# Optimization experiments

Hardware: AMD Instinct MI355X
Metric: run time of the kernel (lower is better)

The kernel has to match this reference:

```python
import jax, jax.numpy as jnp
import numpy as np

VOCAB, EMB, HID, LAYERS = 50000, 128, 128, 3
B, T = 4096, 50


def gru_layer(x, Wih, Whh, bih, bhh):
    """PyTorch-convention GRU over time-major x: [T, B, D] -> [T, B, H]."""
    H = Whh.shape[1]
    h0 = jnp.zeros((x.shape[1], H), x.dtype)
    gi_all = jnp.einsum('tbd,gd->tbg', x, Wih) + bih  # precompute input gates [T,B,3H]

    def step(h, gi):
        gh = h @ Whh.T + bhh
        i_r, i_z, i_n = jnp.split(gi, 3, axis=-1)
        h_r, h_z, h_n = jnp.split(gh, 3, axis=-1)
        r = jax.nn.sigmoid(i_r + h_r)
        z = jax.nn.sigmoid(i_z + h_z)
        n = jnp.tanh(i_n + r * h_n)
        h_new = (1.0 - z) * n + z * h
        return h_new, h_new

    _, ys = jax.lax.scan(step, h0, gi_all)
    return ys


def drnn(x, params):
    """Dilated RNN stack (zalandoresearch DRNN): dilation 2^l per layer.
    x: [B, T, E] -> [B, T, H]."""
    h = jnp.swapaxes(x, 0, 1)  # time-major [T, B, D]
    for l, (Wih, Whh, bih, bhh) in enumerate(params):
        rate = 2 ** l
        Tn, Bn, Dn = h.shape
        Tp = ((Tn + rate - 1) // rate) * rate
        hp = jnp.pad(h, ((0, Tp - Tn), (0, 0), (0, 0)))
        # interleave: dilated[t', j*B:(j+1)*B] = hp[t'*rate + j]
        hd = hp.reshape(Tp // rate, rate * Bn, Dn)
        od = gru_layer(hd, Wih, Whh, bih, bhh)  # [Tp/rate, rate*B, H]
        h = od.reshape(Tp, Bn, -1)[:Tn]
    return jnp.swapaxes(h, 0, 1)  # [B, T, H]


def setup_inputs() -> dict:
    key = jax.random.key(0)
    ks = jax.random.split(key, 2 + 4 * LAYERS)
    inp = {}
    inp['text_inputs'] = jax.random.randint(ks[0], (B, T), 0, VOCAB)
    inp['mask_input'] = (inp['text_inputs'] > 0).astype(jnp.int32)
    inp['len_seq'] = inp['mask_input'].sum(axis=1)
    inp['emb'] = jax.random.normal(ks[1], (VOCAB, EMB), jnp.float32) * 0.02
    s = 1.0 / np.sqrt(HID)
    for l in range(LAYERS):
        din = EMB if l == 0 else HID
        k0, k1, k2, k3 = ks[2 + 4 * l], ks[3 + 4 * l], ks[4 + 4 * l], ks[5 + 4 * l]
        inp[f'Wih{l}'] = jax.random.uniform(k0, (3 * HID, din), jnp.float32, -s, s)
        inp[f'Whh{l}'] = jax.random.uniform(k1, (3 * HID, HID), jnp.float32, -s, s)
        inp[f'bih{l}'] = jax.random.uniform(k2, (3 * HID,), jnp.float32, -s, s)
        inp[f'bhh{l}'] = jax.random.uniform(k3, (3 * HID,), jnp.float32, -s, s)
    return inp


def reference(text_inputs, mask_input, len_seq, emb,
              Wih0, Whh0, bih0, bhh0,
              Wih1, Whh1, bih1, bhh1,
              Wih2, Whh2, bih2, bhh2):
    params = [(Wih0, Whh0, bih0, bhh0),
              (Wih1, Whh1, bih1, bhh1),
              (Wih2, Whh2, bih2, bhh2)]
    x = emb[text_inputs]                       # [B, T, E]
    lens = jnp.sign(text_inputs).sum(axis=1)   # recomputed mask lengths
    order = jnp.argsort(-lens)                 # sort descending by length
    inv = jnp.argsort(order)                   # inverse permutation
    out = drnn(x[order], params)[inv]          # [B, T, H]
    sent_mask = (lens > 0).astype(out.dtype)   # zero out empty sentences
    return out * sent_mask[:, None, None]
```

## Files before the change

### kernel.cpp

```cpp
#include <hip/hip_runtime.h>
#include <hip/hip_bf16.h>
#include <hip/hip_fp16.h>
#include <math.h>


#define B_N 4096
#define T_N 50
#define H_N 128

typedef _Float16 half8 __attribute__((ext_vector_type(8)));
typedef float f32x4 __attribute__((ext_vector_type(4)));

__global__ void prep_weights_kernel(const float* __restrict__ Wih,
                                    const float* __restrict__ Whh,
                                    const float* __restrict__ bih,
                                    const float* __restrict__ bhh,
                                    _Float16* __restrict__ Wp,
                                    float* __restrict__ biasP) {
  const int g = blockIdx.x;
  const int k = threadIdx.x;
  Wp[g * H_N + k]         = (_Float16)Wih[(size_t)g * H_N + k];
  Wp[49152 + g * H_N + k] = (_Float16)Whh[(size_t)g * H_N + k];
  if (k == 0) {
    if (g < 256) biasP[g] = bih[g] + bhh[g];
    else { biasP[g] = bih[g]; biasP[g + 128] = bhh[g]; }
  }
}

__global__ void gather_kernel(const int* __restrict__ tok,
                              const float* __restrict__ emb,
                              _Float16* __restrict__ X0) {
  const int tid = threadIdx.x;
  const int r   = blockIdx.x * 16 + (tid >> 4);
  const int t   = r >> 12;
  const int b   = r & (B_N - 1);
  const int c8  = (tid & 15) * 8;
  const int tk  = tok[b * T_N + t];
  const float4* ep = (const float4*)(emb + (size_t)tk * H_N + c8);
  const float4 a = ep[0], d = ep[1];
  half8 v = { (_Float16)a.x, (_Float16)a.y, (_Float16)a.z, (_Float16)a.w,
              (_Float16)d.x, (_Float16)d.y, (_Float16)d.z, (_Float16)d.w };
  *(half8*)(X0 + (size_t)r * H_N + c8) = v;
}

__global__ void mask_kernel(const int* __restrict__ tok, float* __restrict__ mask) {
  const int b = blockIdx.x * 256 + threadIdx.x;
  int any = 0;
  for (int t = 0; t < T_N; ++t) any |= tok[b * T_N + t];
  mask[b] = any ? 1.0f : 0.0f;
}

__device__ __forceinline__ float sigm(float x) {
  return 1.0f / (1.0f + __expf(-x));
}
__device__ __forceinline__ float tanh_fast(float x) {
  x = fminf(fmaxf(x, -15.0f), 15.0f);
  const float t = __expf(2.0f * x);
  return (t - 1.0f) / (t + 1.0f);
}

template <int RATE, int TSTEPS, bool LAST>
__global__ __launch_bounds__(512, 2) void gru_mfma_kernel(
    const _Float16* __restrict__ X, void* __restrict__ Yv,
    const _Float16* __restrict__ Wp, const float* __restrict__ biasP,
    const float* __restrict__ maskF) {
  __shared__ _Float16 hs[2][16][136];

  const int tid  = threadIdx.x;
  const int lane = tid & 63;
  const int w    = tid >> 6;
  const int cb   = w * 16;
  const int l15  = lane & 15;
  const int lq   = lane >> 4;
  const int c    = cb + l15;

  {
    _Float16* hp = &hs[0][0][0];
    for (int i = tid; i < 16 * 136; i += 512) hp[i] = (_Float16)0.f;
  }

  half8 Wf[3][4], Uf[3][4];
#pragma unroll
  for (int g = 0; g < 3; ++g)
#pragma unroll
    for (int kc = 0; kc < 4; ++kc) {
      const size_t off = (size_t)(g * H_N + c) * H_N + kc * 32 + lq * 8;
      Wf[g][kc] = *(const half8*)(Wp + off);
      Uf[g][kc] = *(const half8*)(Wp + 49152 + off);
    }

  const float br = biasP[c],       bz = biasP[128 + c];
  const float bi = biasP[256 + c], bh = biasP[384 + c];
  float hold[4] = {0.f, 0.f, 0.f, 0.f};

  const int d0 = blockIdx.x * 16;

  half8 xc[4], xn[4];
  {
    const _Float16* xp = X + ((size_t)d0 + l15) * H_N + lq * 8;
#pragma unroll
    for (int kc = 0; kc < 4; ++kc) xc[kc] = *(const half8*)(xp + kc * 32);
  }
  __syncthreads();

  for (int tp = 0; tp < TSTEPS; ++tp) {
    const int cur = tp & 1, nxt = cur ^ 1;

    {
      const int tn = (tp + 1 < TSTEPS) ? tp + 1 : tp;
      const _Float16* xp =
          X + ((size_t)tn * RATE * B_N + d0 + l15) * H_N + lq * 8;
#pragma unroll
      for (int kc = 0; kc < 4; ++kc) xn[kc] = *(const half8*)(xp + kc * 32);
    }

    half8 hf[4];
#pragma unroll
    for (int kc = 0; kc < 4; ++kc)
      hf[kc] = *(const half8*)(&hs[cur][l15][kc * 32 + lq * 8]);

    f32x4 ar  = {br, br, br, br}, az  = {bz, bz, bz, bz};
    f32x4 ani = {bi, bi, bi, bi}, anh = {bh, bh, bh, bh};
#pragma unroll
    for (int kc = 0; kc < 4; ++kc) {
      ar  = __builtin_amdgcn_mfma_f32_16x16x32_f16(xc[kc], Wf[0][kc], ar,  0, 0, 0);
      az  = __builtin_amdgcn_mfma_f32_16x16x32_f16(xc[kc], Wf[1][kc], az,  0, 0, 0);
      ani = __builtin_amdgcn_mfma_f32_16x16x32_f16(xc[kc], Wf[2][kc], ani, 0, 0, 0);
      ar  = __builtin_amdgcn_mfma_f32_16x16x32_f16(hf[kc], Uf[0][kc], ar,  0, 0, 0);
      az  = __builtin_amdgcn_mfma_f32_16x16x32_f16(hf[kc], Uf[1][kc], az,  0, 0, 0);
      anh = __builtin_amdgcn_mfma_f32_16x16x32_f16(hf[kc], Uf[2][kc], anh, 0, 0, 0);
    }

#pragma unroll
    for (int j = 0; j < 4; ++j) {
      const int crow = lq * 4 + j;
      const float rr = sigm(ar[j]);
      const float zz = sigm(az[j]);
      const float nn = tanh_fast(ani[j] + rr * anh[j]);
      const float hv = nn + zz * (hold[j] - nn);
      hold[j] = hv;

      const _Float16 hhalf = (_Float16)hv;
      const unsigned short hb = __builtin_bit_cast(unsigned short, hhalf);
      const unsigned int other =
          (unsigned short)__shfl_xor((int)hb, 1, 64);
      const unsigned int packed = (unsigned int)hb | (other << 16);

      if (!(lane & 1))
        *(unsigned int*)(&hs[nxt][crow][c]) = packed;

      if (!LAST) {
        if (!(lane & 1)) {
          const size_t row_g = (size_t)tp * RATE * B_N + d0 + crow;
          *(unsigned int*)((_Float16*)Yv + row_g * H_N + c) = packed;
        }
      } else {
        const int d = d0 + crow;
        const int t = tp * RATE + (d >> 12);
        if (t < T_N) {
          const int b = d & (B_N - 1);
          ((float*)Yv)[((size_t)b * T_N + t) * H_N + c] = hv * maskF[b];
        }
      }
    }

#pragma unroll
    for (int kc = 0; kc < 4; ++kc) xc[kc] = xn[kc];
    __syncthreads();
  }
}

extern "C" void kernel_launch(void* const* d_in, const int* in_sizes, int n_in,
                              void* d_out, int out_size, void* d_ws, size_t ws_size,
                              hipStream_t stream) {
  (void)in_sizes; (void)n_in; (void)out_size; (void)ws_size;
  const int*   tok = (const int*)d_in[0];
  const float* emb = (const float*)d_in[3];

  char* ws = (char*)d_ws;
  const size_t XBYTES = (size_t)212992 * H_N * 2;
  _Float16* X0    = (_Float16*)ws;
  _Float16* X1    = (_Float16*)(ws + XBYTES);
  _Float16* Wp    = (_Float16*)(ws + 2 * XBYTES);
  float*    biasP = (float*)(ws + 2 * XBYTES + 3 * 196608);
  float*    maskF = biasP + 3 * 512;

  for (int l = 0; l < 3; ++l) {
    const float* Wih = (const float*)d_in[4 + 4 * l];
    const float* Whh = (const float*)d_in[5 + 4 * l];
    const float* bih = (const float*)d_in[6 + 4 * l];
    const float* bhh = (const float*)d_in[7 + 4 * l];
    prep_weights_kernel<<<384, 128, 0, stream>>>(Wih, Whh, bih, bhh,
                                                 Wp + (size_t)l * 98304,
                                                 biasP + l * 512);
  }
  gather_kernel<<<12800, 256, 0, stream>>>(tok, emb, X0);
  mask_kernel<<<16, 256, 0, stream>>>(tok, maskF);
  hipMemsetAsync(X0 + (size_t)204800 * H_N, 0,
                 (size_t)(212992 - 204800) * H_N * 2, stream);

  gru_mfma_kernel<1, 50, false><<<256, 512, 0, stream>>>(
      X0, X1, Wp, biasP, maskF);
  gru_mfma_kernel<2, 25, false><<<512, 512, 0, stream>>>(
      X1, X0, Wp + 98304, biasP + 512, maskF);
  gru_mfma_kernel<4, 13, true><<<1024, 512, 0, stream>>>(
      X0, (float*)d_out, Wp + 2 * 98304, biasP + 1024, maskF);
}
```

Baseline: 464.1 us.

## Store activations and weights in MFMA fragment layout, batch input projections per 4 steps

Weights and activations are pre-swizzled into MFMA fragment order so each lane loads a contiguous half8, and the recurrent weights are staged in LDS (about 104 KB dynamic shared memory) instead of registers. The input projection for four timesteps is computed in one batch before the sequential recurrence, which moves it off the serial critical path and frees registers. The cost is more LDS traffic per step for U fragments, lower occupancy from the large LDS allocation, and scalar 16-bit stores for h.

After: 530.5 us. +14.3%, slower.

```diff
diff --git a/kernel.cpp b/kernel.cpp
--- a/kernel.cpp
+++ b/kernel.cpp
@@ -11,16 +11,23 @@
 typedef _Float16 half8 __attribute__((ext_vector_type(8)));
 typedef float f32x4 __attribute__((ext_vector_type(4)));
 
+#define MFMA16(a, b, c) __builtin_amdgcn_mfma_f32_16x16x32_f16((a), (b), (c), 0, 0, 0)
+
 __global__ void prep_weights_kernel(const float* __restrict__ Wih,
                                     const float* __restrict__ Whh,
                                     const float* __restrict__ bih,
                                     const float* __restrict__ bhh,
-                                    _Float16* __restrict__ Wp,
+                                    _Float16* __restrict__ WihF,
+                                    _Float16* __restrict__ WhhF,
                                     float* __restrict__ biasP) {
   const int g = blockIdx.x;
   const int k = threadIdx.x;
-  Wp[g * H_N + k]         = (_Float16)Wih[(size_t)g * H_N + k];
-  Wp[49152 + g * H_N + k] = (_Float16)Whh[(size_t)g * H_N + k];
+  const int gate = g >> 7, c = g & 127;
+  const int wv = c >> 4, kc = k >> 5;
+  const int lane = (c & 15) | (((k >> 3) & 3) << 4);
+  const int idx = ((wv * 12 + gate * 4 + kc) * 64 + lane) * 8 + (k & 7);
+  WihF[idx] = (_Float16)Wih[(size_t)g * H_N + k];
+  WhhF[idx] = (_Float16)Whh[(size_t)g * H_N + k];
   if (k == 0) {
     if (g < 256) biasP[g] = bih[g] + bhh[g];
     else { biasP[g] = bih[g]; biasP[g + 128] = bhh[g]; }
@@ -29,18 +36,21 @@
 
 __global__ void gather_kernel(const int* __restrict__ tok,
                               const float* __restrict__ emb,
-                              _Float16* __restrict__ X0) {
-  const int tid = threadIdx.x;
-  const int r   = blockIdx.x * 16 + (tid >> 4);
-  const int t   = r >> 12;
-  const int b   = r & (B_N - 1);
-  const int c8  = (tid & 15) * 8;
-  const int tk  = tok[b * T_N + t];
+                              _Float16* __restrict__ XF) {
+  const int p    = blockIdx.x;
+  const int tid  = threadIdx.x;
+  const int kc   = tid >> 6;
+  const int lane = tid & 63;
+  const int row  = p * 16 + (lane & 15);
+  const int t    = row >> 12;
+  const int b    = row & (B_N - 1);
+  const int c8   = kc * 32 + (lane >> 4) * 8;
+  const int tk   = tok[b * T_N + t];
   const float4* ep = (const float4*)(emb + (size_t)tk * H_N + c8);
   const float4 a = ep[0], d = ep[1];
   half8 v = { (_Float16)a.x, (_Float16)a.y, (_Float16)a.z, (_Float16)a.w,
               (_Float16)d.x, (_Float16)d.y, (_Float16)d.z, (_Float16)d.w };
-  *(half8*)(X0 + (size_t)r * H_N + c8) = v;
+  *(half8*)(XF + (((size_t)p * 4 + kc) * 64 + lane) * 8) = v;
 }
 
 __global__ void mask_kernel(const int* __restrict__ tok, float* __restrict__ mask) {
@@ -61,114 +71,121 @@
 
 template <int RATE, int TSTEPS, bool LAST>
 __global__ __launch_bounds__(512, 2) void gru_mfma_kernel(
-    const _Float16* __restrict__ X, void* __restrict__ Yv,
-    const _Float16* __restrict__ Wp, const float* __restrict__ biasP,
-    const float* __restrict__ maskF) {
-  __shared__ _Float16 hs[2][16][136];
+    const _Float16* __restrict__ XF, void* __restrict__ Yv,
+    const _Float16* __restrict__ WihF, const _Float16* __restrict__ WhhF,
+    const float* __restrict__ biasP, const float* __restrict__ maskF) {
+  extern __shared__ _Float16 lds[];
+  _Float16* Ul  = lds;
+  _Float16* hsl = lds + 49152;
 
   const int tid  = threadIdx.x;
   const int lane = tid & 63;
   const int w    = tid >> 6;
-  const int cb   = w * 16;
   const int l15  = lane & 15;
   const int lq   = lane >> 4;
-  const int c    = cb + l15;
-
-  {
-    _Float16* hp = &hs[0][0][0];
-    for (int i = tid; i < 16 * 136; i += 512) hp[i] = (_Float16)0.f;
-  }
-
-  half8 Wf[3][4], Uf[3][4];
-#pragma unroll
-  for (int g = 0; g < 3; ++g)
-#pragma unroll
-    for (int kc = 0; kc < 4; ++kc) {
-      const size_t off = (size_t)(g * H_N + c) * H_N + kc * 32 + lq * 8;
-      Wf[g][kc] = *(const half8*)(Wp + off);
-      Uf[g][kc] = *(const half8*)(Wp + 49152 + off);
-    }
+  const int c    = (w << 4) + l15;
+  const int d0   = blockIdx.x << 4;
+
+  for (int i = tid; i < 6144; i += 512)
+    *(half8*)(Ul + i * 8) = *(const half8*)(WhhF + (size_t)i * 8);
+  for (int i = tid; i < 512; i += 512)
+    *(half8*)(hsl + i * 8) = half8{0,0,0,0,0,0,0,0};
 
   const float br = biasP[c],       bz = biasP[128 + c];
   const float bi = biasP[256 + c], bh = biasP[384 + c];
+  float mkv[4];
+#pragma unroll
+  for (int j = 0; j < 4; ++j)
+    mkv[j] = LAST ? maskF[(d0 & (B_N - 1)) + lq * 4 + j] : 0.0f;
+
   float hold[4] = {0.f, 0.f, 0.f, 0.f};
-
-  const int d0 = blockIdx.x * 16;
-
-  half8 xc[4], xn[4];
-  {
-    const _Float16* xp = X + ((size_t)d0 + l15) * H_N + lq * 8;
-#pragma unroll
-    for (int kc = 0; kc < 4; ++kc) xc[kc] = *(const half8*)(xp + kc * 32);
-  }
   __syncthreads();
 
-  for (int tp = 0; tp < TSTEPS; ++tp) {
-    const int cur = tp & 1, nxt = cur ^ 1;
-
-    {
-      const int tn = (tp + 1 < TSTEPS) ? tp + 1 : tp;
-      const _Float16* xp =
-          X + ((size_t)tn * RATE * B_N + d0 + l15) * H_N + lq * 8;
-#pragma unroll
-      for (int kc = 0; kc < 4; ++kc) xn[kc] = *(const half8*)(xp + kc * 32);
+  int cur = 0;
+  for (int tp0 = 0; tp0 < TSTEPS; tp0 += 4) {
+    const int bs = (TSTEPS - tp0 < 4) ? (TSTEPS - tp0) : 4;
+
+    f32x4 gr[4], gz[4], gn[4];
+#pragma unroll
+    for (int s = 0; s < 4; ++s) {
+      gr[s] = f32x4{br, br, br, br};
+      gz[s] = f32x4{bz, bz, bz, bz};
+      gn[s] = f32x4{bi, bi, bi, bi};
     }
-
-    half8 hf[4];
-#pragma unroll
-    for (int kc = 0; kc < 4; ++kc)
-      hf[kc] = *(const half8*)(&hs[cur][l15][kc * 32 + lq * 8]);
-
-    f32x4 ar  = {br, br, br, br}, az  = {bz, bz, bz, bz};
-    f32x4 ani = {bi, bi, bi, bi}, anh = {bh, bh, bh, bh};
 #pragma unroll
     for (int kc = 0; kc < 4; ++kc) {
-      ar  = __builtin_amdgcn_mfma_f32_16x16x32_f16(xc[kc], Wf[0][kc], ar,  0, 0, 0);
-      az  = __builtin_amdgcn_mfma_f32_16x16x32_f16(xc[kc], Wf[1][kc], az,  0, 0, 0);
-      ani = __builtin_amdgcn_mfma_f32_16x16x32_f16(xc[kc], Wf[2][kc], ani, 0, 0, 0);
-      ar  = __builtin_amdgcn_mfma_f32_16x16x32_f16(hf[kc], Uf[0][kc], ar,  0, 0, 0);
-      az  = __builtin_amdgcn_mfma_f32_16x16x32_f16(hf[kc], Uf[1][kc], az,  0, 0, 0);
-      anh = __builtin_amdgcn_mfma_f32_16x16x32_f16(hf[kc], Uf[2][kc], anh, 0, 0, 0);
-    }
-
-#pragma unroll
-    for (int j = 0; j < 4; ++j) {
-      const int crow = lq * 4 + j;
-      const float rr = sigm(ar[j]);
-      const float zz = sigm(az[j]);
-      const float nn = tanh_fast(ani[j] + rr * anh[j]);
-      const float hv = nn + zz * (hold[j] - nn);
-      hold[j] = hv;
-
-      const _Float16 hhalf = (_Float16)hv;
-      const unsigned short hb = __builtin_bit_cast(unsigned short, hhalf);
-      const unsigned int other =
-          (unsigned short)__shfl_xor((int)hb, 1, 64);
-      const unsigned int packed = (unsigned int)hb | (other << 16);
-
-      if (!(lane & 1))
-        *(unsigned int*)(&hs[nxt][crow][c]) = packed;
-
-      if (!LAST) {
-        if (!(lane & 1)) {
-          const size_t row_g = (size_t)tp * RATE * B_N + d0 + crow;
-          *(unsigned int*)((_Float16*)Yv + row_g * H_N + c) = packed;
-        }
-      } else {
-        const int d = d0 + crow;
-        const int t = tp * RATE + (d >> 12);
-        if (t < T_N) {
-          const int b = d & (B_N - 1);
-          ((float*)Yv)[((size_t)b * T_N + t) * H_N + c] = hv * maskF[b];
+      const int wf = (w * 12 + kc) * 64 + lane;
+      const half8 wr = *(const half8*)(WihF + (size_t)(wf      ) * 8);
+      const half8 wz = *(const half8*)(WihF + (size_t)(wf + 256) * 8);
+      const half8 wn = *(const half8*)(WihF + (size_t)(wf + 512) * 8);
+#pragma unroll
+      for (int s = 0; s < 4; ++s) {
+        if (s < bs) {
+          const size_t panel = (size_t)(tp0 + s) * RATE * 256 + blockIdx.x;
+          const half8 xv =
+              *(const half8*)(XF + ((panel * 4 + kc) * 64 + lane) * 8);
+          gr[s] = MFMA16(xv, wr, gr[s]);
+          gz[s] = MFMA16(xv, wz, gz[s]);
+          gn[s] = MFMA16(xv, wn, gn[s]);
         }
       }
     }
 
 #pragma unroll
-    for (int kc = 0; kc < 4; ++kc) xc[kc] = xn[kc];
-    __syncthreads();
+    for (int s = 0; s < 4; ++s) {
+      if (s < bs) {
+        const int tp = tp0 + s;
+        half8 hf[4];
+#pragma unroll
+        for (int kc = 0; kc < 4; ++kc)
+          hf[kc] = *(const half8*)(hsl + cur * 2048 + (kc * 64 + lane) * 8);
+
+        f32x4 ar = gr[s], az = gz[s], an = gn[s];
+        f32x4 ah = f32x4{bh, bh, bh, bh};
+#pragma unroll
+        for (int kc = 0; kc < 4; ++kc) {
+          const int uf = (w * 12 + kc) * 64 + lane;
+          const half8 ur = *(const half8*)(Ul + (uf      ) * 8);
+          const half8 uz = *(const half8*)(Ul + (uf + 256) * 8);
+          const half8 un = *(const half8*)(Ul + (uf + 512) * 8);
+          ar = MFMA16(hf[kc], ur, ar);
+          az = MFMA16(hf[kc], uz, az);
+          ah = MFMA16(hf[kc], un, ah);
+        }
+
+        const int nxt = cur ^ 1;
+#pragma unroll
+        for (int j = 0; j < 4; ++j) {
+          const int crow = lq * 4 + j;
+          const float rr = sigm(ar[j]);
+          const float zz = sigm(az[j]);
+          const float nn = tanh_fast(an[j] + rr * ah[j]);
+          const float hv = nn + zz * (hold[j] - nn);
+          hold[j] = hv;
+          const _Float16 hh = (_Float16)hv;
+          const int hidx = ((c >> 5) * 64 + crow + ((c >> 3) & 3) * 16) * 8
+                           + (c & 7);
+          hsl[nxt * 2048 + hidx] = hh;
+          if (!LAST) {
+            const size_t panel = (size_t)tp * RATE * 256 + blockIdx.x;
+            ((_Float16*)Yv)[panel * 2048 + hidx] = hh;
+          } else {
+            const int d = d0 + crow;
+            const int t = tp * RATE + (d >> 12);
+            if (t < T_N) {
+              const int b = d & (B_N - 1);
+              ((float*)Yv)[((size_t)b * T_N + t) * H_N + c] = hv * mkv[j];
+            }
+          }
+        }
+        cur ^= 1;
+        __syncthreads();
+      }
+    }
   }
 }
+
+#define LDS_BYTES 106496
 
 extern "C" void kernel_launch(void* const* d_in, const int* in_sizes, int n_in,
                               void* d_out, int out_size, void* d_ws, size_t ws_size,
@@ -179,30 +196,36 @@
 
   char* ws = (char*)d_ws;
   const size_t XBYTES = (size_t)212992 * H_N * 2;
-  _Float16* X0    = (_Float16*)ws;
-  _Float16* X1    = (_Float16*)(ws + XBYTES);
-  _Float16* Wp    = (_Float16*)(ws + 2 * XBYTES);
-  float*    biasP = (float*)(ws + 2 * XBYTES + 3 * 196608);
+  _Float16* X0   = (_Float16*)ws;
+  _Float16* X1   = (_Float16*)(ws + XBYTES);
+  _Float16* WihF = (_Float16*)(ws + 2 * XBYTES);
+  _Float16* WhhF = WihF + 3 * 49152;
+  float*    biasP = (float*)(WhhF + 3 * 49152);
   float*    maskF = biasP + 3 * 512;
 
   for (int l = 0; l < 3; ++l) {
-    const float* Wih = (const float*)d_in[4 + 4 * l];
-    const float* Whh = (const float*)d_in[5 + 4 * l];
-    const float* bih = (const float*)d_in[6 + 4 * l];
-    const float* bhh = (const float*)d_in[7 + 4 * l];
-    prep_weights_kernel<<<384, 128, 0, stream>>>(Wih, Whh, bih, bhh,
-                                                 Wp + (size_t)l * 98304,
-                                                 biasP + l * 512);
+    prep_weights_kernel<<<384, 128, 0, stream>>>(
+        (const float*)d_in[4 + 4 * l], (const float*)d_in[5 + 4 * l],
+        (const float*)d_in[6 + 4 * l], (const float*)d_in[7 + 4 * l],
+        WihF + (size_t)l * 49152, WhhF + (size_t)l * 49152, biasP + l * 512);
   }
   gather_kernel<<<12800, 256, 0, stream>>>(tok, emb, X0);
   mask_kernel<<<16, 256, 0, stream>>>(tok, maskF);
   hipMemsetAsync(X0 + (size_t)204800 * H_N, 0,
                  (size_t)(212992 - 204800) * H_N * 2, stream);
 
-  gru_mfma_kernel<1, 50, false><<<256, 512, 0, stream>>>(
-      X0, X1, Wp, biasP, maskF);
-  gru_mfma_kernel<2, 25, false><<<512, 512, 0, stream>>>(
-      X1, X0, Wp + 98304, biasP + 512, maskF);
-  gru_mfma_kernel<4, 13, true><<<1024, 512, 0, stream>>>(
-      X0, (float*)d_out, Wp + 2 * 98304, biasP + 1024, maskF);
-}
+  hipFuncSetAttribute((const void*)&gru_mfma_kernel<1, 50, false>,
+                      hipFuncAttributeMaxDynamicSharedMemorySize, LDS_BYTES);
+  hipFuncSetAttribute((const void*)&gru_mfma_kernel<2, 25, false>,
+                      hipFuncAttributeMaxDynamicSharedMemorySize, LDS_BYTES);
+  hipFuncSetAttribute((const void*)&gru_mfma_kernel<4, 13, true>,
+                      hipFuncAttributeMaxDynamicSharedMemorySize, LDS_BYTES);
+
+  gru_mfma_kernel<1, 50, false><<<256, 512, LDS_BYTES, stream>>>(
+      X0, X1, WihF, WhhF, biasP, maskF);
+  gru_mfma_kernel<2, 25, false><<<512, 512, LDS_BYTES, stream>>>(
+      X1, X0, WihF + 49152, WhhF + 49152, biasP + 512, maskF);
+  gru_mfma_kernel<4, 13, true><<<1024, 512, LDS_BYTES, stream>>>(
+      X0, (float*)d_out, WihF + 2 * 49152, WhhF + 2 * 49152,
+      biasP + 1024, maskF);
+}
```
